# Kernel optimization log

Measured on AMD Instinct MI355X. Metric: run time of the kernel, lower is better.

## Reference

```python
import jax, jax.numpy as jnp
import numpy as np

# 8 trilerp corners in (x, y, z) component order, matching the original's
# [floor/ceil] enumeration: fff, ffc, fcf, fcc, cff, cfc, ccf, ccc.
CORNERS = np.array([[0, 0, 0], [0, 0, 1], [0, 1, 0], [0, 1, 1],
                    [1, 0, 0], [1, 0, 1], [1, 1, 0], [1, 1, 1]], dtype=np.int32)

N = 32768          # number of points
NUM_KERNELS = 4    # submodels
GRID = 16          # voxel grid size
C_IN = 64          # input_channels
C_OUT = 64         # features


def setup_inputs() -> dict:
    key = jax.random.key(0)
    k1, k2, k3, k4, k5 = jax.random.split(key, 5)
    param_idxs = jax.random.randint(k1, (N, 1), 0, NUM_KERNELS, dtype=jnp.int32)
    pos = jax.random.uniform(k2, (N, 3), dtype=jnp.float32)
    xs = jax.random.normal(k3, (N, C_IN), dtype=jnp.float32)
    # he_uniform over fan_in = input_channels
    limit = np.sqrt(6.0 / C_IN).astype(np.float32)
    kernels = jax.random.uniform(
        k4, (NUM_KERNELS, GRID, GRID, GRID, C_IN, C_OUT),
        dtype=jnp.float32, minval=-limit, maxval=limit)
    biases = jnp.zeros((NUM_KERNELS, GRID, GRID, GRID, C_OUT), dtype=jnp.float32)
    return {"param_idxs": param_idxs, "pos": pos, "xs": xs,
            "kernels": kernels, "biases": biases}


def reference(param_idxs, pos, xs, kernels, biases):
    """Trilinearly-interpolated per-point dense layer.

    Equivalent to building kernel = sum_c w_c * K_c and computing x @ kernel + bias;
    by linearity we accumulate w_c * (x @ K_c + b_c) directly, avoiding the
    materialized per-point interpolated kernel.
    """
    grid = kernels.shape[1]
    pidx = param_idxs.reshape(-1)            # (N,)
    loc = pos * grid - 0.5                    # (N, 3)
    floored = jnp.floor(loc)
    ceil_w = loc - floored                    # trilerp weights toward ceil
    floor_w = 1.0 - ceil_w
    out = jnp.zeros((pos.shape[0], kernels.shape[-1]), dtype=xs.dtype)
    for corner in CORNERS:                    # fixed 8-iteration loop
        idx = jnp.clip((floored + corner).astype(jnp.int32), 0, grid - 1)  # (N,3)
        w = jnp.prod(jnp.where(corner[None, :] == 1, ceil_w, floor_w), axis=-1)  # (N,)
        # Original indexes kernels[pidx, z, y, x] with z=idx[:,2], y=idx[:,1], x=idx[:,0]
        gk = kernels[pidx, idx[:, 2], idx[:, 1], idx[:, 0]]  # (N, C_in, C_out)
        gb = biases[pidx, idx[:, 2], idx[:, 1], idx[:, 0]]   # (N, C_out)
        out = out + w[:, None] * (jnp.einsum('nc,ncf->nf', xs, gk) + gb)
    return out
```

## Files before the change

kernel.cpp:

```cpp
#include <hip/hip_runtime.h>
#include <math.h>

#define NPTS   32768
#define NK     4
#define GRID   16
#define CIN    64
#define COUT   64
#define NCELLS (NK*GRID*GRID*GRID)
#define NENT   (NPTS*8)

typedef __attribute__((ext_vector_type(8))) short  short8;
typedef __attribute__((ext_vector_type(4))) float  f32x4;

static __device__ inline unsigned short f2bf(float f) {
    unsigned int u = __builtin_bit_cast(unsigned int, f);
    unsigned int r = u + 0x7fff + ((u >> 16) & 1);
    return (unsigned short)(r >> 16);
}

__global__ void k_hist(const int* __restrict__ pidx, const float* __restrict__ pos,
                       int* __restrict__ hist, int n) {
    int p = blockIdx.x * blockDim.x + threadIdx.x;
    if (p >= n) return;
    int pk = pidx[p];
    float lx = pos[3*p+0]*16.f - 0.5f;
    float ly = pos[3*p+1]*16.f - 0.5f;
    float lz = pos[3*p+2]*16.f - 0.5f;
    int fx = (int)floorf(lx), fy = (int)floorf(ly), fz = (int)floorf(lz);
#pragma unroll
    for (int c = 0; c < 8; ++c) {
        int c0 = c & 1, c1 = (c >> 1) & 1, c2 = (c >> 2) & 1;
        int ix = min(max(fx + c0, 0), GRID-1);
        int iy = min(max(fy + c1, 0), GRID-1);
        int iz = min(max(fz + c2, 0), GRID-1);
        int cell = ((pk*GRID + iz)*GRID + iy)*GRID + ix;
        atomicAdd(&hist[cell], 1);
    }
}

__global__ void k_alloc(const int* __restrict__ hist, int* __restrict__ offsets,
                        int* __restrict__ cursor, int* __restrict__ gcnt) {
    int i = blockIdx.x * blockDim.x + threadIdx.x;
    int l = threadIdx.x & 63;
    int v = hist[i];
    int p = v;
#pragma unroll
    for (int d = 1; d < 64; d <<= 1) {
        int t = __shfl_up(p, d);
        if (l >= d) p += t;
    }
    int total = __shfl(p, 63);
    int base = 0;
    if (l == 63) base = atomicAdd(gcnt, total);
    base = __shfl(base, 63);
    int off = base + p - v;
    offsets[i] = off;
    cursor[i]  = off;
}

__global__ void k_scatter(const int* __restrict__ pidx, const float* __restrict__ pos,
                          int* __restrict__ cursor, int* __restrict__ epid,
                          float* __restrict__ ew, int n) {
    int p = blockIdx.x * blockDim.x + threadIdx.x;
    if (p >= n) return;
    int pk = pidx[p];
    float lx = pos[3*p+0]*16.f - 0.5f;
    float ly = pos[3*p+1]*16.f - 0.5f;
    float lz = pos[3*p+2]*16.f - 0.5f;
    float flx = floorf(lx), fly = floorf(ly), flz = floorf(lz);
    int fx = (int)flx, fy = (int)fly, fz = (int)flz;
    float tx = lx - flx, ty = ly - fly, tz = lz - flz;
    float wx[2] = {1.f - tx, tx};
    float wy[2] = {1.f - ty, ty};
    float wz[2] = {1.f - tz, tz};
#pragma unroll
    for (int c = 0; c < 8; ++c) {
        int c0 = c & 1, c1 = (c >> 1) & 1, c2 = (c >> 2) & 1;
        int ix = min(max(fx + c0, 0), GRID-1);
        int iy = min(max(fy + c1, 0), GRID-1);
        int iz = min(max(fz + c2, 0), GRID-1);
        int cell = ((pk*GRID + iz)*GRID + iy)*GRID + ix;
        float w = wx[c0] * wy[c1] * wz[c2];
        int e = atomicAdd(&cursor[cell], 1);
        epid[e] = p;
        ew[e]   = w;
    }
}

__global__ __launch_bounds__(256)
void k_main(const float* __restrict__ xs, const float* __restrict__ kernels,
            const float* __restrict__ biases, const int* __restrict__ offsets,
            const int* __restrict__ hist, const int* __restrict__ epid,
            const float* __restrict__ ew, float* __restrict__ out) {
    __shared__ unsigned short Ks[CIN * COUT];
    __shared__ unsigned short Xb[16 * 72];
    __shared__ float wB[16];
    __shared__ int   pB[16];

    int cell  = blockIdx.x;
    int start = offsets[cell];
    int cnt   = hist[cell];
    if (cnt == 0) return;
    int end = start + cnt;

    int tid = threadIdx.x;
    int l   = tid & 63;
    int wv  = tid >> 6;
    int m16 = l & 15;
    int q   = l >> 4;

    const float* Kg = kernels + (size_t)cell * (CIN * COUT);
    {
#pragma unroll
        for (int r = 0; r < 4; ++r) {
            int j = r * 1024 + tid * 4;
            float4 kv = *(const float4*)&Kg[j];
            ushort4 kb = { f2bf(kv.x), f2bf(kv.y), f2bf(kv.z), f2bf(kv.w) };
            *(ushort4*)&Ks[j] = kb;
        }
    }
    __syncthreads();

    int ncol = wv * 16 + m16;
    short8 Bf[2];
#pragma unroll
    for (int s = 0; s < 2; ++s) {
#pragma unroll
        for (int j = 0; j < 8; ++j) {
            Bf[s][j] = (short)Ks[(s * 32 + q * 8 + j) * COUT + ncol];
        }
    }
    float bias_c = biases[(size_t)cell * COUT + ncol];

    int nb = (cnt + 15) >> 4;
    for (int b = 0; b < nb; ++b) {
        {
            int row = tid >> 4;
            int c4  = (tid & 15) << 2;
            int e   = start + (b << 4) + row;
            int pid = (e < end) ? epid[e] : 0;
            float4 xv = *(const float4*)&xs[(size_t)pid * CIN + c4];
            ushort4 xb = { f2bf(xv.x), f2bf(xv.y), f2bf(xv.z), f2bf(xv.w) };
            *(ushort4*)&Xb[row * 72 + c4] = xb;
            if (tid < 16) {
                int e2 = start + (b << 4) + tid;
                bool valid = e2 < end;
                pB[tid] = valid ? epid[e2] : 0;
                wB[tid] = valid ? ew[e2] : 0.f;
            }
        }
        __syncthreads();

        f32x4 acc = {0.f, 0.f, 0.f, 0.f};
#pragma unroll
        for (int s = 0; s < 2; ++s) {
            const short8 af = *(const short8*)&Xb[m16 * 72 + s * 32 + q * 8];
            acc = __builtin_amdgcn_mfma_f32_16x16x32_bf16(af, Bf[s], acc, 0, 0, 0);
        }

#pragma unroll
        for (int reg = 0; reg < 4; ++reg) {
            int row = q * 4 + reg;
            float w = wB[row];
            if (w != 0.f) {
                int pid = pB[row];
                float val = w * (acc[reg] + bias_c);
                unsafeAtomicAdd(&out[(size_t)pid * COUT + ncol], val);
            }
        }
        __syncthreads();
    }
}

extern "C" void kernel_launch(void* const* d_in, const int* in_sizes, int n_in,
                              void* d_out, int out_size, void* d_ws, size_t ws_size,
                              hipStream_t stream) {
    const int*   pidx    = (const int*)  d_in[0];
    const float* pos     = (const float*)d_in[1];
    const float* xs      = (const float*)d_in[2];
    const float* kernels = (const float*)d_in[3];
    const float* biases  = (const float*)d_in[4];
    float*       out     = (float*)d_out;
    int n = in_sizes[0];

    int* ws      = (int*)d_ws;
    int* hist    = ws;
    int* gcnt    = ws + NCELLS;
    int* offsets = ws + NCELLS + 16;
    int* cursor  = offsets + NCELLS;
    int* epid    = cursor + NCELLS;
    float* ew    = (float*)(epid + NENT);

    hipMemsetAsync(hist, 0, (NCELLS + 16) * sizeof(int), stream);
    hipMemsetAsync(d_out, 0, (size_t)out_size * sizeof(float), stream);

    int blocks = (n + 255) / 256;
    k_hist   <<<blocks,       256, 0, stream>>>(pidx, pos, hist, n);
    k_alloc  <<<NCELLS / 256, 256, 0, stream>>>(hist, offsets, cursor, gcnt);
    k_scatter<<<blocks,       256, 0, stream>>>(pidx, pos, cursor, epid, ew, n);
    k_main   <<<NCELLS,       256, 0, stream>>>(xs, kernels, biases, offsets,
                                                hist, epid, ew, out);
}
```

Before: 422.6 us.

## Process 16 cells per block with double-buffered async LDS kernel loads

Each block of the main kernel now handles 16 consecutive cells instead of one. The next cell's fp32 weights are prefetched into a second LDS buffer with global_load_lds while the current cell is computed, so the large weight stream overlaps with MMA work. Point features are loaded straight into MFMA A registers rather than staged through shared memory, which removes per-batch barriers. Per-cell segments are padded to multiples of 16 so the point-id and weight metadata can be read with vector loads. The trade-offs are a larger workspace, uninitialized padding entries that rely on masking, and far fewer blocks, which lowers the available parallelism.

```diff
diff --git a/kernel.cpp b/kernel.cpp
--- a/kernel.cpp
+++ b/kernel.cpp
@@ -3,11 +3,13 @@
 
 #define NPTS   32768
 #define NK     4
-#define GRID   16
+#define GRID_  16
 #define CIN    64
 #define COUT   64
-#define NCELLS (NK*GRID*GRID*GRID)
+#define NCELLS (NK*GRID_*GRID_*GRID_)
 #define NENT   (NPTS*8)
+#define NENTP  (NENT + NCELLS*15)
+#define CPB    16
 
 typedef __attribute__((ext_vector_type(8))) short  short8;
 typedef __attribute__((ext_vector_type(4))) float  f32x4;
@@ -30,10 +32,10 @@
 #pragma unroll
     for (int c = 0; c < 8; ++c) {
         int c0 = c & 1, c1 = (c >> 1) & 1, c2 = (c >> 2) & 1;
-        int ix = min(max(fx + c0, 0), GRID-1);
-        int iy = min(max(fy + c1, 0), GRID-1);
-        int iz = min(max(fz + c2, 0), GRID-1);
-        int cell = ((pk*GRID + iz)*GRID + iy)*GRID + ix;
+        int ix = min(max(fx + c0, 0), GRID_-1);
+        int iy = min(max(fy + c1, 0), GRID_-1);
+        int iz = min(max(fz + c2, 0), GRID_-1);
+        int cell = ((pk*GRID_ + iz)*GRID_ + iy)*GRID_ + ix;
         atomicAdd(&hist[cell], 1);
     }
 }
@@ -42,8 +44,9 @@
                         int* __restrict__ cursor, int* __restrict__ gcnt) {
     int i = blockIdx.x * blockDim.x + threadIdx.x;
     int l = threadIdx.x & 63;
-    int v = hist[i];
-    int p = v;
+    int v  = hist[i];
+    int vp = (v + 15) & ~15;
+    int p = vp;
 #pragma unroll
     for (int d = 1; d < 64; d <<= 1) {
         int t = __shfl_up(p, d);
@@ -53,7 +56,7 @@
     int base = 0;
     if (l == 63) base = atomicAdd(gcnt, total);
     base = __shfl(base, 63);
-    int off = base + p - v;
+    int off = base + p - vp;
     offsets[i] = off;
     cursor[i]  = off;
 }
@@ -76,10 +79,10 @@
 #pragma unroll
     for (int c = 0; c < 8; ++c) {
         int c0 = c & 1, c1 = (c >> 1) & 1, c2 = (c >> 2) & 1;
-        int ix = min(max(fx + c0, 0), GRID-1);
-        int iy = min(max(fy + c1, 0), GRID-1);
-        int iz = min(max(fz + c2, 0), GRID-1);
-        int cell = ((pk*GRID + iz)*GRID + iy)*GRID + ix;
+        int ix = min(max(fx + c0, 0), GRID_-1);
+        int iy = min(max(fy + c1, 0), GRID_-1);
+        int iz = min(max(fz + c2, 0), GRID_-1);
+        int cell = ((pk*GRID_ + iz)*GRID_ + iy)*GRID_ + ix;
         float w = wx[c0] * wy[c1] * wz[c2];
         int e = atomicAdd(&cursor[cell], 1);
         epid[e] = p;
@@ -92,83 +95,86 @@
             const float* __restrict__ biases, const int* __restrict__ offsets,
             const int* __restrict__ hist, const int* __restrict__ epid,
             const float* __restrict__ ew, float* __restrict__ out) {
-    __shared__ unsigned short Ks[CIN * COUT];
-    __shared__ unsigned short Xb[16 * 72];
-    __shared__ float wB[16];
-    __shared__ int   pB[16];
-
-    int cell  = blockIdx.x;
-    int start = offsets[cell];
-    int cnt   = hist[cell];
-    if (cnt == 0) return;
-    int end = start + cnt;
-
+    __shared__ float Ks[2][CIN * COUT];
     int tid = threadIdx.x;
     int l   = tid & 63;
     int wv  = tid >> 6;
     int m16 = l & 15;
     int q   = l >> 4;
-
-    const float* Kg = kernels + (size_t)cell * (CIN * COUT);
+    int cell0 = blockIdx.x * CPB;
+    int ncol  = wv * 16 + m16;
+
     {
+        const float* Kg = kernels + (size_t)cell0 * (CIN * COUT);
 #pragma unroll
         for (int r = 0; r < 4; ++r) {
-            int j = r * 1024 + tid * 4;
-            float4 kv = *(const float4*)&Kg[j];
-            ushort4 kb = { f2bf(kv.x), f2bf(kv.y), f2bf(kv.z), f2bf(kv.w) };
-            *(ushort4*)&Ks[j] = kb;
-        }
-    }
-    __syncthreads();
-
-    int ncol = wv * 16 + m16;
-    short8 Bf[2];
-#pragma unroll
-    for (int s = 0; s < 2; ++s) {
+            int off = ((r * 4 + wv) * 64 + l) * 4;
+            __builtin_amdgcn_global_load_lds(
+                (const __attribute__((address_space(1))) void*)(Kg + off),
+                (__attribute__((address_space(3))) void*)(&Ks[0][off]), 16, 0, 0);
+        }
+    }
+
+    for (int ci = 0; ci < CPB; ++ci) {
+        int cur = ci & 1;
+        __syncthreads();
+        if (ci + 1 < CPB) {
+            const float* Kg = kernels + (size_t)(cell0 + ci + 1) * (CIN * COUT);
+#pragma unroll
+            for (int r = 0; r < 4; ++r) {
+                int off = ((r * 4 + wv) * 64 + l) * 4;
+                __builtin_amdgcn_global_load_lds(
+                    (const __attribute__((address_space(1))) void*)(Kg + off),
+                    (__attribute__((address_space(3))) void*)(&Ks[1 - cur][off]), 16, 0, 0);
+            }
+        }
+        int cell = cell0 + ci;
+        int cnt  = hist[cell];
+        if (cnt == 0) continue;
+        int start = offsets[cell];
+
+        short8 Bf0, Bf1;
 #pragma unroll
         for (int j = 0; j < 8; ++j) {
-            Bf[s][j] = (short)Ks[(s * 32 + q * 8 + j) * COUT + ncol];
-        }
-    }
-    float bias_c = biases[(size_t)cell * COUT + ncol];
-
-    int nb = (cnt + 15) >> 4;
-    for (int b = 0; b < nb; ++b) {
-        {
-            int row = tid >> 4;
-            int c4  = (tid & 15) << 2;
-            int e   = start + (b << 4) + row;
-            int pid = (e < end) ? epid[e] : 0;
-            float4 xv = *(const float4*)&xs[(size_t)pid * CIN + c4];
-            ushort4 xb = { f2bf(xv.x), f2bf(xv.y), f2bf(xv.z), f2bf(xv.w) };
-            *(ushort4*)&Xb[row * 72 + c4] = xb;
-            if (tid < 16) {
-                int e2 = start + (b << 4) + tid;
-                bool valid = e2 < end;
-                pB[tid] = valid ? epid[e2] : 0;
-                wB[tid] = valid ? ew[e2] : 0.f;
+            Bf0[j] = (short)f2bf(Ks[cur][(q * 8 + j) * COUT + ncol]);
+            Bf1[j] = (short)f2bf(Ks[cur][(32 + q * 8 + j) * COUT + ncol]);
+        }
+        float bias_c = biases[(size_t)cell * COUT + ncol];
+
+        int nb = (cnt + 15) >> 4;
+        for (int b = 0; b < nb; ++b) {
+            int ebase = start + (b << 4);
+            int pidA = epid[ebase + m16] & (NPTS - 1);
+            const float* xr = xs + (size_t)pidA * CIN + q * 8;
+            float4 a0 = *(const float4*)(xr);
+            float4 a1 = *(const float4*)(xr + 4);
+            float4 a2 = *(const float4*)(xr + 32);
+            float4 a3 = *(const float4*)(xr + 36);
+            short8 af0, af1;
+            af0[0]=(short)f2bf(a0.x); af0[1]=(short)f2bf(a0.y);
+            af0[2]=(short)f2bf(a0.z); af0[3]=(short)f2bf(a0.w);
+            af0[4]=(short)f2bf(a1.x); af0[5]=(short)f2bf(a1.y);
+            af0[6]=(short)f2bf(a1.z); af0[7]=(short)f2bf(a1.w);
+            af1[0]=(short)f2bf(a2.x); af1[1]=(short)f2bf(a2.y);
+            af1[2]=(short)f2bf(a2.z); af1[3]=(short)f2bf(a2.w);
+            af1[4]=(short)f2bf(a3.x); af1[5]=(short)f2bf(a3.y);
+            af1[6]=(short)f2bf(a3.z); af1[7]=(short)f2bf(a3.w);
+
+            f32x4 acc = {0.f, 0.f, 0.f, 0.f};
+            acc = __builtin_amdgcn_mfma_f32_16x16x32_bf16(af0, Bf0, acc, 0, 0, 0);
+            acc = __builtin_amdgcn_mfma_f32_16x16x32_bf16(af1, Bf1, acc, 0, 0, 0);
+
+            int erow = ebase + (q << 2);
+            int4   pe = *(const int4*)&epid[erow];
+            float4 we = *(const float4*)&ew[erow];
+            int rem = cnt - (b << 4) - (q << 2);
+            if (rem > 0) {
+                unsafeAtomicAdd(&out[(size_t)(pe.x) * COUT + ncol], we.x * (acc[0] + bias_c));
+                if (rem > 1) unsafeAtomicAdd(&out[(size_t)(pe.y) * COUT + ncol], we.y * (acc[1] + bias_c));
+                if (rem > 2) unsafeAtomicAdd(&out[(size_t)(pe.z) * COUT + ncol], we.z * (acc[2] + bias_c));
+                if (rem > 3) unsafeAtomicAdd(&out[(size_t)(pe.w) * COUT + ncol], we.w * (acc[3] + bias_c));
             }
         }
-        __syncthreads();
-
-        f32x4 acc = {0.f, 0.f, 0.f, 0.f};
-#pragma unroll
-        for (int s = 0; s < 2; ++s) {
-            const short8 af = *(const short8*)&Xb[m16 * 72 + s * 32 + q * 8];
-            acc = __builtin_amdgcn_mfma_f32_16x16x32_bf16(af, Bf[s], acc, 0, 0, 0);
-        }
-
-#pragma unroll
-        for (int reg = 0; reg < 4; ++reg) {
-            int row = q * 4 + reg;
-            float w = wB[row];
-            if (w != 0.f) {
-                int pid = pB[row];
-                float val = w * (acc[reg] + bias_c);
-                unsafeAtomicAdd(&out[(size_t)pid * COUT + ncol], val);
-            }
-        }
-        __syncthreads();
     }
 }
 
@@ -189,7 +195,7 @@
     int* offsets = ws + NCELLS + 16;
     int* cursor  = offsets + NCELLS;
     int* epid    = cursor + NCELLS;
-    float* ew    = (float*)(epid + NENT);
+    float* ew    = (float*)(epid + NENTP);
 
     hipMemsetAsync(hist, 0, (NCELLS + 16) * sizeof(int), stream);
     hipMemsetAsync(d_out, 0, (size_t)out_size * sizeof(float), stream);
@@ -198,6 +204,6 @@
     k_hist   <<<blocks,       256, 0, stream>>>(pidx, pos, hist, n);
     k_alloc  <<<NCELLS / 256, 256, 0, stream>>>(hist, offsets, cursor, gcnt);
     k_scatter<<<blocks,       256, 0, stream>>>(pidx, pos, cursor, epid, ew, n);
-    k_main   <<<NCELLS,       256, 0, stream>>>(xs, kernels, biases, offsets,
+    k_main   <<<NCELLS / CPB, 256, 0, stream>>>(xs, kernels, biases, offsets,
                                                 hist, epid, ew, out);
 }
```

After: 442.0 us. 1.05x slower.
